# Performance work log

Hardware: AMD Instinct MI355X
Metric: run time of the kernel (lower is better)

Reference implementation:

```python
import jax, jax.numpy as jnp
import numpy as np

NUM_GROUPS1 = 8
NUM_GROUPS2 = 4
NUM_HEADS = 8


def setup_inputs() -> dict:
    key = jax.random.key(0)
    k1, k2, k3 = jax.random.split(key, 3)
    B, N, C = 8, 4096, 512
    x = jax.random.normal(k1, (B, N, C), dtype=jnp.float32)
    # torch Linear(dim, 3*inner_dim, bias=False); stored transposed for x @ W
    W_qkv = jax.random.normal(k2, (C, 3 * C), dtype=jnp.float32) * 0.02
    W_proj = jax.random.normal(k3, (C, C), dtype=jnp.float32) * 0.02
    b_proj = jnp.zeros((C,), dtype=jnp.float32)
    return {"x": x, "W_qkv": W_qkv, "W_proj": W_proj, "b_proj": b_proj,
            "recursive_index": 0}


def reference(x, W_qkv, W_proj, b_proj, recursive_index):
    # recursive_index is a static Python int (0 -> False branch, num_groups1).
    num_groups = NUM_GROUPS1 if not recursive_index else NUM_GROUPS2
    B, N, C = x.shape
    H = NUM_HEADS
    Dh = C // H
    scale = Dh ** -0.5
    Np = int(np.ceil(N / num_groups) * num_groups)
    if Np != N:
        x = jnp.pad(x, ((0, 0), (0, Np - N), (0, 0)))
    L = Np // num_groups  # tokens per group
    # qkv projection, then split into per-group per-head tensors [B,G,H,L,Dh]
    qkv = (x @ W_qkv).reshape(B, num_groups, L, 3, H, Dh)
    q = jnp.transpose(qkv[:, :, :, 0], (0, 1, 3, 2, 4))
    k = jnp.transpose(qkv[:, :, :, 1], (0, 1, 3, 2, 4))
    v = jnp.transpose(qkv[:, :, :, 2], (0, 1, 3, 2, 4))
    attn = jax.nn.softmax(jnp.einsum('bghld,bghmd->bghlm', q, k) * scale, axis=-1)
    out = jnp.einsum('bghlm,bghmd->bghld', attn, v)  # [B,G,H,L,Dh]
    out = jnp.transpose(out, (0, 1, 3, 2, 4)).reshape(B, Np, C)[:, :N]
    return out @ W_proj + b_proj
```

## Files before the change

kernel.cpp:

```cpp
#include <hip/hip_runtime.h>
#include <hip/hip_bf16.h>

typedef __attribute__((ext_vector_type(8))) short  bf16x8;
typedef __attribute__((ext_vector_type(4))) float  f32x4;

__device__ __forceinline__ ushort f2bf(float f) {
    unsigned u = __builtin_bit_cast(unsigned, f);
    u += 0x7fffu + ((u >> 16) & 1u);
    return (ushort)(u >> 16);
}

__device__ __forceinline__ void gload_lds16(const ushort* g, ushort* l) {
    __builtin_amdgcn_global_load_lds(
        (const __attribute__((address_space(1))) void*)(g),
        (__attribute__((address_space(3))) void*)(l), 16, 0, 0);
}

__global__ __launch_bounds__(256) void prep_kernel(
        const float* __restrict__ x, ushort* __restrict__ xb,
        const float* __restrict__ Wqkv, ushort* __restrict__ wq,
        const float* __restrict__ Wproj, ushort* __restrict__ wp) {
    __shared__ ushort t[64 * 65];
    const int bx = blockIdx.x, tid = threadIdx.x;
    if (bx < 16384) {
        int i = bx * 256 + tid;
        float4 f = reinterpret_cast<const float4*>(x)[i];
        ushort4 o;
        o.x = f2bf(f.x); o.y = f2bf(f.y); o.z = f2bf(f.z); o.w = f2bf(f.w);
        reinterpret_cast<ushort4*>(xb)[i] = o;
        return;
    }
    const float* in; ushort* out; int Cc, qcols, cB, rB; float qs;
    if (bx < 16576) {
        int b2 = bx - 16384;
        in = Wqkv; out = wq; Cc = 1536; qcols = 512;
        qs = 0.18033688011112043f;
        cB = (b2 % 24) * 64; rB = (b2 / 24) * 64;
    } else {
        int b2 = bx - 16576;
        in = Wproj; out = wp; Cc = 512; qcols = 0; qs = 1.0f;
        cB = (b2 % 8) * 64; rB = (b2 / 8) * 64;
    }
#pragma unroll
    for (int p = 0; p < 16; ++p) {
        int lin = p * 256 + tid;
        int r = lin >> 6, c = lin & 63;
        float v = in[(size_t)(rB + r) * Cc + cB + c];
        if (cB + c < qcols) v *= qs;
        t[c * 65 + r] = f2bf(v);
    }
    __syncthreads();
#pragma unroll
    for (int p = 0; p < 16; ++p) {
        int lin = p * 256 + tid;
        int c = lin >> 6, r = lin & 63;
        out[(size_t)(cB + c) * 512 + rB + r] = t[c * 65 + r];
    }
}

template<bool F32OUT, bool EMIT_VT>
__global__ __launch_bounds__(256) void gemm_bt_kernel(
        const ushort* __restrict__ A, const ushort* __restrict__ Bt,
        void* __restrict__ Cout, const float* __restrict__ bias,
        ushort* __restrict__ vT, int Ncols, int K) {
    __shared__ ushort smem[9216];
    ushort* la = smem;
    ushort* lb = smem + 4096;
    const int tid  = threadIdx.x;
    const int id = blockIdx.x;
    const int mBase = ((id & 7) * 32 + ((id >> 3) & 31)) << 7;
    const int nBase = (id >> 8) << 7;
    const int w = tid >> 6, lane = tid & 63, ml = lane & 15, quad = lane >> 4;
    const int wr = (w >> 1) << 6, wc = (w & 1) << 6;

    const int srow   = lane >> 2;
    const int schunk = (lane & 3) ^ (srow & 3) ^ ((srow >> 2) & 3);
    const ushort* Ap = A + (size_t)(mBase + w * 32 + srow) * K + schunk * 8;
    const ushort* Bp = Bt + (size_t)(nBase + w * 32 + srow) * K + schunk * 8;
    ushort* lA0 = la + (w * 32) * 32;
    ushort* lB0 = lb + (w * 32) * 32;

    f32x4 z4 = {0.f, 0.f, 0.f, 0.f};
    f32x4 acc[4][4];
#pragma unroll
    for (int i = 0; i < 4; ++i)
#pragma unroll
        for (int j = 0; j < 4; ++j) acc[i][j] = z4;

    const int sx = ((quad ^ (ml & 3) ^ ((ml >> 2) & 3)) << 3);
    const int nkt = K >> 5;
    for (int kt = 0; kt < nkt; ++kt) {
        gload_lds16(Ap,          lA0);
        gload_lds16(Ap + 16 * K, lA0 + 16 * 32);
        gload_lds16(Bp,          lB0);
        gload_lds16(Bp + 16 * K, lB0 + 16 * 32);
        Ap += 32; Bp += 32;
        __syncthreads();
        bf16x8 af[4], bv[4];
#pragma unroll
        for (int i = 0; i < 4; ++i)
            af[i] = *reinterpret_cast<bf16x8*>(la + (wr + i * 16 + ml) * 32 + sx);
#pragma unroll
        for (int j = 0; j < 4; ++j)
            bv[j] = *reinterpret_cast<bf16x8*>(lb + (wc + j * 16 + ml) * 32 + sx);
#pragma unroll
        for (int i = 0; i < 4; ++i)
#pragma unroll
            for (int j = 0; j < 4; ++j)
                acc[i][j] = __builtin_amdgcn_mfma_f32_16x16x32_bf16(af[i], bv[j], acc[i][j], 0, 0, 0);
        __syncthreads();
    }

    if (F32OUT) {
        float* ep = reinterpret_cast<float*>(smem) + w * 1088;
        float bj[4];
#pragma unroll
        for (int j = 0; j < 4; ++j) bj[j] = bias[nBase + wc + j * 16 + ml];
        float* cbase = reinterpret_cast<float*>(Cout);
#pragma unroll
        for (int i = 0; i < 4; ++i) {
#pragma unroll
            for (int j = 0; j < 4; ++j)
#pragma unroll
                for (int r = 0; r < 4; ++r)
                    ep[(quad * 4 + r) * 68 + j * 16 + ml] = acc[i][j][r] + bj[j];
#pragma unroll
            for (int t = 0; t < 4; ++t) {
                int ch = quad + 4 * t;
                float4 v = *reinterpret_cast<const float4*>(ep + ml * 68 + ch * 4);
                *reinterpret_cast<float4*>(cbase
                    + (size_t)(mBase + wr + i * 16 + ml) * Ncols + nBase + wc + ch * 4) = v;
            }
        }
    } else if (!EMIT_VT || nBase < 1024) {
        ushort* ep = smem + w * 1152;
#pragma unroll
        for (int i = 0; i < 4; ++i) {
#pragma unroll
            for (int j = 0; j < 4; ++j)
#pragma unroll
                for (int r = 0; r < 4; ++r)
                    ep[(quad * 4 + r) * 72 + j * 16 + ml] = f2bf(acc[i][j][r]);
#pragma unroll
            for (int t = 0; t < 2; ++t) {
                int ch = quad + 4 * t;
                bf16x8 v = *reinterpret_cast<const bf16x8*>(ep + ml * 72 + ch * 8);
                *reinterpret_cast<bf16x8*>(reinterpret_cast<ushort*>(Cout)
                    + (size_t)(mBase + wr + i * 16 + ml) * Ncols + nBase + wc + ch * 8) = v;
            }
        }
    } else {
#pragma unroll
        for (int p = 0; p < 2; ++p) {
            if ((w >> 1) == p) {
                ushort* ep = smem + (w & 1) * 4608;
#pragma unroll
                for (int i = 0; i < 4; ++i)
#pragma unroll
                    for (int j = 0; j < 4; ++j)
#pragma unroll
                        for (int r = 0; r < 4; ++r)
                            ep[(j * 16 + ml) * 72 + i * 16 + quad * 4 + r] = f2bf(acc[i][j][r]);
                const int tok0 = mBase + wr;
                const int grp  = tok0 >> 9, tokin = tok0 & 511;
#pragma unroll
                for (int pass = 0; pass < 8; ++pass) {
                    int dl = pass * 8 + (lane >> 3), ch = lane & 7;
                    bf16x8 v = *reinterpret_cast<const bf16x8*>(ep + dl * 72 + ch * 8);
                    int vg = (nBase - 1024) + wc + dl;
                    *reinterpret_cast<bf16x8*>(vT
                        + ((size_t)(grp * 512 + vg)) * 512 + tokin + ch * 8) = v;
                }
            }
            __syncthreads();
        }
    }
}

__global__ __launch_bounds__(256) void attn_kernel(
        const ushort* __restrict__ qk, const ushort* __restrict__ vT,
        ushort* __restrict__ out) {
    __shared__ ushort k_lds[32 * 64];
    __shared__ ushort v_lds[64 * 32];
    __shared__ ushort p_lds[4 * 32 * 40];
    const int tid = threadIdx.x;
    const int w = tid >> 6, lane = tid & 63, ml = lane & 15, quad = lane >> 4;
    const int id = blockIdx.x;
    const int bgh = id >> 2, qc = id & 3;
    const int b = bgh >> 6, g = (bgh >> 3) & 7, h = bgh & 7;
    const int tb = b * 4096 + g * 512;
    const ushort* base  = qk + (size_t)tb * 1024 + h * 64;
    const ushort* vbase = vT + ((size_t)((b * 8 + g) * 512 + h * 64)) * 512;
    const int qOff = qc * 128 + w * 32;

    bf16x8 qf[2][2];
#pragma unroll
    for (int qb = 0; qb < 2; ++qb)
#pragma unroll
        for (int ks = 0; ks < 2; ++ks)
            qf[qb][ks] = *reinterpret_cast<const bf16x8*>(
                base + (size_t)(qOff + qb * 16 + ml) * 1024 + ks * 32 + quad * 8);

    const int krl = lane >> 3;
    const int kch = (lane & 7) ^ krl;
    const ushort* kp = base + (size_t)(w * 8 + krl) * 1024 + 512 + kch * 8;
    ushort* kdst = k_lds + (w * 8) * 64;
    const int vrl = lane >> 2;
    const int vch = (lane & 3) ^ (vrl & 3) ^ ((vrl >> 2) & 3);
    const ushort* vp = vbase + (size_t)(w * 16 + vrl) * 512 + vch * 8;
    ushort* vdst = v_lds + (w * 16) * 32;

    f32x4 z4 = {0.f, 0.f, 0.f, 0.f};
    f32x4 oacc[2][4];
    float lp[2];
#pragma unroll
    for (int qb = 0; qb < 2; ++qb) {
#pragma unroll
        for (int db = 0; db < 4; ++db) oacc[qb][db] = z4;
        lp[qb] = 0.f;
    }

    const int ksw = ml & 7;
    const int vsw = (ml & 3) ^ ((ml >> 2) & 3);
    ushort* pw = p_lds + w * 32 * 40;
    for (int kt = 0; kt < 16; ++kt) {
        gload_lds16(kp + (size_t)kt * 32 * 1024, kdst);
        gload_lds16(vp + kt * 32, vdst);
        __syncthreads();

        bf16x8 kf[2][2];
#pragma unroll
        for (int kb = 0; kb < 2; ++kb)
#pragma unroll
            for (int ks = 0; ks < 2; ++ks)
                kf[kb][ks] = *reinterpret_cast<bf16x8*>(
                    k_lds + (kb * 16 + ml) * 64 + (((ks * 4 + quad) ^ ksw) << 3));
        f32x4 s[2][2];
#pragma unroll
        for (int qb = 0; qb < 2; ++qb)
#pragma unroll
            for (int kb = 0; kb < 2; ++kb) {
                f32x4 t = z4;
                t = __builtin_amdgcn_mfma_f32_16x16x32_bf16(kf[kb][0], qf[qb][0], t, 0, 0, 0);
                t = __builtin_amdgcn_mfma_f32_16x16x32_bf16(kf[kb][1], qf[qb][1], t, 0, 0, 0);
                s[qb][kb] = t;
            }

#pragma unroll
        for (int qb = 0; qb < 2; ++qb)
#pragma unroll
            for (int kb = 0; kb < 2; ++kb) {
                float p0 = exp2f(s[qb][kb][0]), p1 = exp2f(s[qb][kb][1]);
                float p2 = exp2f(s[qb][kb][2]), p3 = exp2f(s[qb][kb][3]);
                lp[qb] += (p0 + p1) + (p2 + p3);
                ushort4 pk;
                pk.x = f2bf(p0); pk.y = f2bf(p1); pk.z = f2bf(p2); pk.w = f2bf(p3);
                *reinterpret_cast<ushort4*>(
                    pw + (qb * 16 + ml) * 40 + kb * 16 + quad * 4) = pk;
            }

        bf16x8 pf[2], vf[4];
#pragma unroll
        for (int qb = 0; qb < 2; ++qb)
            pf[qb] = *reinterpret_cast<bf16x8*>(pw + (qb * 16 + ml) * 40 + quad * 8);
#pragma unroll
        for (int db = 0; db < 4; ++db)
            vf[db] = *reinterpret_cast<bf16x8*>(
                v_lds + (db * 16 + ml) * 32 + ((quad ^ vsw) << 3));
#pragma unroll
        for (int qb = 0; qb < 2; ++qb)
#pragma unroll
            for (int db = 0; db < 4; ++db)
                oacc[qb][db] = __builtin_amdgcn_mfma_f32_16x16x32_bf16(pf[qb], vf[db], oacc[qb][db], 0, 0, 0);
        __syncthreads();
    }

    float invq[2][4];
#pragma unroll
    for (int qb = 0; qb < 2; ++qb) {
        float sline = lp[qb];
        sline += __shfl_xor(sline, 16);
        sline += __shfl_xor(sline, 32);
        float rinv = 1.0f / sline;
#pragma unroll
        for (int r = 0; r < 4; ++r)
            invq[qb][r] = __shfl(rinv, quad * 4 + r);
    }
#pragma unroll
    for (int qb = 0; qb < 2; ++qb)
#pragma unroll
        for (int db = 0; db < 4; ++db)
#pragma unroll
            for (int r = 0; r < 4; ++r) {
                float v = oacc[qb][db][r] * invq[qb][r];
                out[(size_t)(tb + qOff + qb * 16 + quad * 4 + r) * 512
                    + h * 64 + db * 16 + ml] = f2bf(v);
            }
}

extern "C" void kernel_launch(void* const* d_in, const int* in_sizes, int n_in,
                              void* d_out, int out_size, void* d_ws, size_t ws_size,
                              hipStream_t stream) {
    const float* x     = (const float*)d_in[0];
    const float* Wqkv  = (const float*)d_in[1];
    const float* Wproj = (const float*)d_in[2];
    const float* bproj = (const float*)d_in[3];

    char* ws = (char*)d_ws;
    ushort* xb   = (ushort*)(ws);
    ushort* wq   = (ushort*)(ws + 33554432);
    ushort* wp   = (ushort*)(ws + 35127296);
    ushort* qkb  = (ushort*)(ws + 35651584);
    ushort* vTb  = (ushort*)(ws + 102760448);
    ushort* attn = xb;
    float*  outp = (float*)d_out;

    prep_kernel<<<16640, 256, 0, stream>>>(x, xb, Wqkv, wq, Wproj, wp);
    gemm_bt_kernel<false, true><<<3072, 256, 0, stream>>>(
        xb, wq, qkb, nullptr, vTb, 1024, 512);
    attn_kernel<<<2048, 256, 0, stream>>>(qkb, vTb, attn);
    gemm_bt_kernel<true, false><<<1024, 256, 0, stream>>>(
        attn, wp, outp, bproj, nullptr, 512, 512);
}
```

Baseline: 314.8 us.

## Double K-tile depth in GEMM and attention; compute V^T directly as Wv·X^T

The GEMM K-step grows from 32 to 64 using an 8-chunk XOR swizzle, which halves the number of barrier-separated iterations. The attention key tile grows from 32 to 64 keys per step, so each step issues more MFMAs per sync. The V-transpose output is now produced by swapping operands (Wv as A, X as B) so blocks write vT rows directly, replacing the two-phase LDS transpose epilogue. LDS use per block rises, which may lower occupancy.

Measured after the change: 298.8 us. 5.1% less time.

```diff
diff --git a/kernel.cpp b/kernel.cpp
--- a/kernel.cpp
+++ b/kernel.cpp
@@ -58,27 +58,38 @@
     }
 }
 
-template<bool F32OUT, bool EMIT_VT>
+template<bool F32OUT, bool SPLIT_VT>
 __global__ __launch_bounds__(256) void gemm_bt_kernel(
         const ushort* __restrict__ A, const ushort* __restrict__ Bt,
         void* __restrict__ Cout, const float* __restrict__ bias,
-        ushort* __restrict__ vT, int Ncols, int K) {
-    __shared__ ushort smem[9216];
+        const ushort* __restrict__ Wv, ushort* __restrict__ vT,
+        int Ncols, int K) {
+    __shared__ ushort smem[16384];
     ushort* la = smem;
-    ushort* lb = smem + 4096;
+    ushort* lb = smem + 8192;
     const int tid  = threadIdx.x;
     const int id = blockIdx.x;
-    const int mBase = ((id & 7) * 32 + ((id >> 3) & 31)) << 7;
-    const int nBase = (id >> 8) << 7;
+    const bool vt = SPLIT_VT && (id >= 2048);
+    const ushort* Amat; const ushort* Bmat; int mBase, nBase;
+    if (!vt) {
+        Amat = A; Bmat = Bt;
+        mBase = ((id & 7) * 32 + ((id >> 3) & 31)) << 7;
+        nBase = (id >> 8) << 7;
+    } else {
+        int vid = id - 2048;
+        Amat = Wv; Bmat = A;
+        mBase = (vid >> 8) << 7;
+        nBase = ((vid & 7) * 32 + ((vid >> 3) & 31)) << 7;
+    }
     const int w = tid >> 6, lane = tid & 63, ml = lane & 15, quad = lane >> 4;
     const int wr = (w >> 1) << 6, wc = (w & 1) << 6;
 
-    const int srow   = lane >> 2;
-    const int schunk = (lane & 3) ^ (srow & 3) ^ ((srow >> 2) & 3);
-    const ushort* Ap = A + (size_t)(mBase + w * 32 + srow) * K + schunk * 8;
-    const ushort* Bp = Bt + (size_t)(nBase + w * 32 + srow) * K + schunk * 8;
-    ushort* lA0 = la + (w * 32) * 32;
-    ushort* lB0 = lb + (w * 32) * 32;
+    const int srow = lane >> 3;
+    const int sch  = (lane & 7) ^ srow;
+    const ushort* Ap = Amat + (size_t)(mBase + w * 32 + srow) * K + sch * 8;
+    const ushort* Bp = Bmat + (size_t)(nBase + w * 32 + srow) * K + sch * 8;
+    ushort* lA0 = la + (w * 32) * 64;
+    ushort* lB0 = lb + (w * 32) * 64;
 
     f32x4 z4 = {0.f, 0.f, 0.f, 0.f};
     f32x4 acc[4][4];
@@ -87,27 +98,32 @@
 #pragma unroll
         for (int j = 0; j < 4; ++j) acc[i][j] = z4;
 
-    const int sx = ((quad ^ (ml & 3) ^ ((ml >> 2) & 3)) << 3);
-    const int nkt = K >> 5;
+    const int nkt = K >> 6;
     for (int kt = 0; kt < nkt; ++kt) {
-        gload_lds16(Ap,          lA0);
-        gload_lds16(Ap + 16 * K, lA0 + 16 * 32);
-        gload_lds16(Bp,          lB0);
-        gload_lds16(Bp + 16 * K, lB0 + 16 * 32);
-        Ap += 32; Bp += 32;
+#pragma unroll
+        for (int i = 0; i < 4; ++i) {
+            gload_lds16(Ap + (size_t)(8 * i) * K, lA0 + (8 * i) * 64);
+            gload_lds16(Bp + (size_t)(8 * i) * K, lB0 + (8 * i) * 64);
+        }
+        Ap += 64; Bp += 64;
         __syncthreads();
-        bf16x8 af[4], bv[4];
-#pragma unroll
-        for (int i = 0; i < 4; ++i)
-            af[i] = *reinterpret_cast<bf16x8*>(la + (wr + i * 16 + ml) * 32 + sx);
-#pragma unroll
-        for (int j = 0; j < 4; ++j)
-            bv[j] = *reinterpret_cast<bf16x8*>(lb + (wc + j * 16 + ml) * 32 + sx);
-#pragma unroll
-        for (int i = 0; i < 4; ++i)
+#pragma unroll
+        for (int ks = 0; ks < 2; ++ks) {
+            bf16x8 af[4], bv[4];
+#pragma unroll
+            for (int i = 0; i < 4; ++i)
+                af[i] = *reinterpret_cast<bf16x8*>(
+                    la + (wr + i * 16 + ml) * 64 + (((ks * 4 + quad) ^ (ml & 7)) << 3));
 #pragma unroll
             for (int j = 0; j < 4; ++j)
-                acc[i][j] = __builtin_amdgcn_mfma_f32_16x16x32_bf16(af[i], bv[j], acc[i][j], 0, 0, 0);
+                bv[j] = *reinterpret_cast<bf16x8*>(
+                    lb + (wc + j * 16 + ml) * 64 + (((ks * 4 + quad) ^ (ml & 7)) << 3));
+#pragma unroll
+            for (int i = 0; i < 4; ++i)
+#pragma unroll
+                for (int j = 0; j < 4; ++j)
+                    acc[i][j] = __builtin_amdgcn_mfma_f32_16x16x32_bf16(af[i], bv[j], acc[i][j], 0, 0, 0);
+        }
         __syncthreads();
     }
 
@@ -132,7 +148,7 @@
                     + (size_t)(mBase + wr + i * 16 + ml) * Ncols + nBase + wc + ch * 4) = v;
             }
         }
-    } else if (!EMIT_VT || nBase < 1024) {
+    } else {
         ushort* ep = smem + w * 1152;
 #pragma unroll
         for (int i = 0; i < 4; ++i) {
@@ -145,34 +161,16 @@
             for (int t = 0; t < 2; ++t) {
                 int ch = quad + 4 * t;
                 bf16x8 v = *reinterpret_cast<const bf16x8*>(ep + ml * 72 + ch * 8);
-                *reinterpret_cast<bf16x8*>(reinterpret_cast<ushort*>(Cout)
-                    + (size_t)(mBase + wr + i * 16 + ml) * Ncols + nBase + wc + ch * 8) = v;
-            }
-        }
-    } else {
-#pragma unroll
-        for (int p = 0; p < 2; ++p) {
-            if ((w >> 1) == p) {
-                ushort* ep = smem + (w & 1) * 4608;
-#pragma unroll
-                for (int i = 0; i < 4; ++i)
-#pragma unroll
-                    for (int j = 0; j < 4; ++j)
-#pragma unroll
-                        for (int r = 0; r < 4; ++r)
-                            ep[(j * 16 + ml) * 72 + i * 16 + quad * 4 + r] = f2bf(acc[i][j][r]);
-                const int tok0 = mBase + wr;
-                const int grp  = tok0 >> 9, tokin = tok0 & 511;
-#pragma unroll
-                for (int pass = 0; pass < 8; ++pass) {
-                    int dl = pass * 8 + (lane >> 3), ch = lane & 7;
-                    bf16x8 v = *reinterpret_cast<const bf16x8*>(ep + dl * 72 + ch * 8);
-                    int vg = (nBase - 1024) + wc + dl;
+                int row = mBase + wr + i * 16 + ml;
+                if (!vt) {
+                    *reinterpret_cast<bf16x8*>(reinterpret_cast<ushort*>(Cout)
+                        + (size_t)row * Ncols + nBase + wc + ch * 8) = v;
+                } else {
                     *reinterpret_cast<bf16x8*>(vT
-                        + ((size_t)(grp * 512 + vg)) * 512 + tokin + ch * 8) = v;
+                        + ((size_t)((nBase >> 9) * 512 + row)) * 512
+                        + (nBase & 511) + wc + ch * 8) = v;
                 }
             }
-            __syncthreads();
         }
     }
 }
@@ -180,9 +178,9 @@
 __global__ __launch_bounds__(256) void attn_kernel(
         const ushort* __restrict__ qk, const ushort* __restrict__ vT,
         ushort* __restrict__ out) {
-    __shared__ ushort k_lds[32 * 64];
-    __shared__ ushort v_lds[64 * 32];
-    __shared__ ushort p_lds[4 * 32 * 40];
+    __shared__ ushort k_lds[64 * 64];
+    __shared__ ushort v_lds[64 * 64];
+    __shared__ ushort p_lds[4 * 32 * 72];
     const int tid = threadIdx.x;
     const int w = tid >> 6, lane = tid & 63, ml = lane & 15, quad = lane >> 4;
     const int id = blockIdx.x;
@@ -201,14 +199,12 @@
             qf[qb][ks] = *reinterpret_cast<const bf16x8*>(
                 base + (size_t)(qOff + qb * 16 + ml) * 1024 + ks * 32 + quad * 8);
 
-    const int krl = lane >> 3;
-    const int kch = (lane & 7) ^ krl;
-    const ushort* kp = base + (size_t)(w * 8 + krl) * 1024 + 512 + kch * 8;
-    ushort* kdst = k_lds + (w * 8) * 64;
-    const int vrl = lane >> 2;
-    const int vch = (lane & 3) ^ (vrl & 3) ^ ((vrl >> 2) & 3);
-    const ushort* vp = vbase + (size_t)(w * 16 + vrl) * 512 + vch * 8;
-    ushort* vdst = v_lds + (w * 16) * 32;
+    const int srow = lane >> 3;
+    const int sch  = (lane & 7) ^ srow;
+    const ushort* kp = base + (size_t)(w * 16 + srow) * 1024 + 512 + sch * 8;
+    ushort* kdst = k_lds + (w * 16) * 64;
+    const ushort* vp = vbase + (size_t)(w * 16 + srow) * 512 + sch * 8;
+    ushort* vdst = v_lds + (w * 16) * 64;
 
     f32x4 z4 = {0.f, 0.f, 0.f, 0.f};
     f32x4 oacc[2][4];
@@ -220,58 +216,63 @@
         lp[qb] = 0.f;
     }
 
-    const int ksw = ml & 7;
-    const int vsw = (ml & 3) ^ ((ml >> 2) & 3);
-    ushort* pw = p_lds + w * 32 * 40;
-    for (int kt = 0; kt < 16; ++kt) {
-        gload_lds16(kp + (size_t)kt * 32 * 1024, kdst);
-        gload_lds16(vp + kt * 32, vdst);
+    ushort* pw = p_lds + w * 32 * 72;
+    for (int kt = 0; kt < 8; ++kt) {
+        gload_lds16(kp + (size_t)(kt * 64) * 1024,     kdst);
+        gload_lds16(kp + (size_t)(kt * 64 + 8) * 1024, kdst + 8 * 64);
+        gload_lds16(vp + kt * 64,           vdst);
+        gload_lds16(vp + 8 * 512 + kt * 64, vdst + 8 * 64);
         __syncthreads();
 
-        bf16x8 kf[2][2];
-#pragma unroll
-        for (int kb = 0; kb < 2; ++kb)
-#pragma unroll
-            for (int ks = 0; ks < 2; ++ks)
-                kf[kb][ks] = *reinterpret_cast<bf16x8*>(
-                    k_lds + (kb * 16 + ml) * 64 + (((ks * 4 + quad) ^ ksw) << 3));
-        f32x4 s[2][2];
+        f32x4 s[2][4];
 #pragma unroll
         for (int qb = 0; qb < 2; ++qb)
 #pragma unroll
-            for (int kb = 0; kb < 2; ++kb) {
-                f32x4 t = z4;
-                t = __builtin_amdgcn_mfma_f32_16x16x32_bf16(kf[kb][0], qf[qb][0], t, 0, 0, 0);
-                t = __builtin_amdgcn_mfma_f32_16x16x32_bf16(kf[kb][1], qf[qb][1], t, 0, 0, 0);
-                s[qb][kb] = t;
-            }
+            for (int kb = 0; kb < 4; ++kb) s[qb][kb] = z4;
+#pragma unroll
+        for (int ks = 0; ks < 2; ++ks) {
+            bf16x8 kfs[4];
+#pragma unroll
+            for (int kb = 0; kb < 4; ++kb)
+                kfs[kb] = *reinterpret_cast<bf16x8*>(
+                    k_lds + (kb * 16 + ml) * 64 + (((ks * 4 + quad) ^ (ml & 7)) << 3));
+#pragma unroll
+            for (int qb = 0; qb < 2; ++qb)
+#pragma unroll
+                for (int kb = 0; kb < 4; ++kb)
+                    s[qb][kb] = __builtin_amdgcn_mfma_f32_16x16x32_bf16(kfs[kb], qf[qb][ks], s[qb][kb], 0, 0, 0);
+        }
 
 #pragma unroll
         for (int qb = 0; qb < 2; ++qb)
 #pragma unroll
-            for (int kb = 0; kb < 2; ++kb) {
+            for (int kb = 0; kb < 4; ++kb) {
                 float p0 = exp2f(s[qb][kb][0]), p1 = exp2f(s[qb][kb][1]);
                 float p2 = exp2f(s[qb][kb][2]), p3 = exp2f(s[qb][kb][3]);
                 lp[qb] += (p0 + p1) + (p2 + p3);
                 ushort4 pk;
                 pk.x = f2bf(p0); pk.y = f2bf(p1); pk.z = f2bf(p2); pk.w = f2bf(p3);
                 *reinterpret_cast<ushort4*>(
-                    pw + (qb * 16 + ml) * 40 + kb * 16 + quad * 4) = pk;
+                    pw + (qb * 16 + ml) * 72 + kb * 16 + quad * 4) = pk;
             }
 
-        bf16x8 pf[2], vf[4];
-#pragma unroll
-        for (int qb = 0; qb < 2; ++qb)
-            pf[qb] = *reinterpret_cast<bf16x8*>(pw + (qb * 16 + ml) * 40 + quad * 8);
-#pragma unroll
-        for (int db = 0; db < 4; ++db)
-            vf[db] = *reinterpret_cast<bf16x8*>(
-                v_lds + (db * 16 + ml) * 32 + ((quad ^ vsw) << 3));
-#pragma unroll
-        for (int qb = 0; qb < 2; ++qb)
+#pragma unroll
+        for (int ks = 0; ks < 2; ++ks) {
+            bf16x8 pfs[2], vfs[4];
+#pragma unroll
+            for (int qb = 0; qb < 2; ++qb)
+                pfs[qb] = *reinterpret_cast<bf16x8*>(
+                    pw + (qb * 16 + ml) * 72 + ks * 32 + quad * 8);
 #pragma unroll
             for (int db = 0; db < 4; ++db)
-                oacc[qb][db] = __builtin_amdgcn_mfma_f32_16x16x32_bf16(pf[qb], vf[db], oacc[qb][db], 0, 0, 0);
+                vfs[db] = *reinterpret_cast<bf16x8*>(
+                    v_lds + (db * 16 + ml) * 64 + (((ks * 4 + quad) ^ (ml & 7)) << 3));
+#pragma unroll
+            for (int qb = 0; qb < 2; ++qb)
+#pragma unroll
+                for (int db = 0; db < 4; ++db)
+                    oacc[qb][db] = __builtin_amdgcn_mfma_f32_16x16x32_bf16(pfs[qb], vfs[db], oacc[qb][db], 0, 0, 0);
+        }
         __syncthreads();
     }
 
@@ -313,12 +314,13 @@
     ushort* qkb  = (ushort*)(ws + 35651584);
     ushort* vTb  = (ushort*)(ws + 102760448);
     ushort* attn = xb;
+    ushort* wv   = wq + 1024 * 512;
     float*  outp = (float*)d_out;
 
     prep_kernel<<<16640, 256, 0, stream>>>(x, xb, Wqkv, wq, Wproj, wp);
     gemm_bt_kernel<false, true><<<3072, 256, 0, stream>>>(
-        xb, wq, qkb, nullptr, vTb, 1024, 512);
+        xb, wq, qkb, nullptr, wv, vTb, 1024, 512);
     attn_kernel<<<2048, 256, 0, stream>>>(qkb, vTb, attn);
     gemm_bt_kernel<true, false><<<1024, 256, 0, stream>>>(
-        attn, wp, outp, bproj, nullptr, 512, 512);
-}
+        attn, wp, outp, bproj, nullptr, nullptr, 512, 512);
+}
```
